# Kernel tuning notes

Hardware: AMD Instinct MI355X
Metric: run time of the kernel (lower is better)

The kernel has to match this reference:

```python
import jax, jax.numpy as jnp
import numpy as np

BS, NR, VDIM, QDIM, CSUB, RDIM = 64, 36, 2048, 1024, 512, 256


def setup_inputs() -> dict:
    key = jax.random.key(0)
    ks = jax.random.split(key, 8)
    s = 0.02  # weight scale
    return {
        "X": jax.random.normal(ks[0], (BS, NR, VDIM), jnp.float32),
        "Q": jax.random.normal(ks[1], (BS, QDIM), jnp.float32),
        "pos": jax.random.uniform(ks[2], (BS, NR, 4), jnp.float32),
        "Wv": jax.random.normal(ks[3], (VDIM + 4, CSUB), jnp.float32) * s,
        "bv": jnp.zeros((CSUB,), jnp.float32),
        "Wq": jax.random.normal(ks[4], (QDIM, CSUB), jnp.float32) * s,
        "bq": jnp.zeros((CSUB,), jnp.float32),
        "W1": jax.random.normal(ks[5], (CSUB, RDIM), jnp.float32) * s,
        "b1": jnp.zeros((RDIM,), jnp.float32),
        "W2": jax.random.normal(ks[6], (RDIM, RDIM), jnp.float32) * s,
        "b2": jnp.zeros((RDIM,), jnp.float32),
    }


def reference(X, Q, pos, Wv, bv, Wq, bq, W1, b1, W2, b2):
    # pe_enable: concat position encodings -> [bs, Nr, v_dim+4]
    Xc = jnp.concatenate([X, pos], axis=-1)
    # FCNet projections (weight-norm linear + ReLU; dropout identity in eval)
    Xp = jax.nn.relu(Xc @ Wv + bv)              # [bs, Nr, C]
    Qp = jax.nn.relu(Q @ Wq + bq)               # [bs, C]
    Xs = Xp + Qp[:, None, :]                    # broadcast question over regions
    # pairwise elementwise product: pair[b,i,j,c] = Xs[b,j,c] * Xs[b,i,c]
    pair = Xs[:, None, :, :] * Xs[:, :, None, :]  # [bs, Nr, Nr, C]
    # 1x1 convs == per-(i,j) channel-mixing matmuls, relu (dropout identity)
    h = jax.nn.relu(jnp.einsum('bijc,cr->bijr', pair, W1) + b1)
    r_emb = jax.nn.relu(jnp.einsum('bijr,rs->bijs', h, W2) + b2)
    return r_emb  # [bs, Nr, Nr, r_dim]
```

## Files before the change

kernel.cpp:

```cpp
#include <hip/hip_runtime.h>
#include <hip/hip_bf16.h>
#include <stdint.h>

#define BSZ 64
#define NRG 36
#define VD  2048
#define QD  1024
#define CS  512
#define RD  256
#define KP  2080
#define MR  (BSZ*NRG)
#define TRI  666
#define TRIQ 768

typedef __bf16 bf16x8 __attribute__((ext_vector_type(8)));
typedef float  f32x4  __attribute__((ext_vector_type(4)));

static __device__ __forceinline__ f32x4 mfma16(bf16x8 a, bf16x8 b, f32x4 c) {
    return __builtin_amdgcn_mfma_f32_16x16x32_bf16(a, b, c, 0, 0, 0);
}

static __device__ __forceinline__ void load_lds16(const __bf16* g, __bf16* l) {
    __builtin_amdgcn_global_load_lds(
        (const __attribute__((address_space(1))) uint32_t*)(const void*)g,
        (__attribute__((address_space(3))) uint32_t*)(void*)l,
        16, 0, 0);
}

__global__ __launch_bounds__(256) void k_prep(
    const float* __restrict__ X, const float* __restrict__ pos,
    const float* __restrict__ Wv, const float* __restrict__ W1,
    const float* __restrict__ W2,
    __bf16* __restrict__ Xc, __bf16* __restrict__ Wvg,
    __bf16* __restrict__ W1g, __bf16* __restrict__ W2g,
    int* __restrict__ lut)
{
    int id = blockIdx.x;
    if (id < MR) {
        const float* xr = X + (size_t)id * VD;
        const float* pr = pos + (size_t)id * 4;
        __bf16* o = Xc + (size_t)id * KP;
        for (int c = threadIdx.x; c < KP; c += 256) {
            float v = 0.f;
            if (c < VD) v = xr[c];
            else if (c < VD + 4) v = pr[c - VD];
            o[c] = (__bf16)v;
        }
        return;
    }
    id -= MR;
    if (id < 520 + 64 + 32) {
        const float* W; __bf16* Wg; int K, N, nbx;
        if (id < 520)      {          W = Wv; Wg = Wvg; K = VD + 4; N = CS; nbx = CS / 64; }
        else if (id < 584) { id -= 520; W = W1; Wg = W1g; K = CS;     N = RD; nbx = RD / 64; }
        else               { id -= 584; W = W2; Wg = W2g; K = RD;     N = RD; nbx = RD / 64; }
        int bx = id % nbx, by = id / nbx;
        int g = by * 4 + (threadIdx.x >> 6);
        int n = bx * 64 + (threadIdx.x & 63);
        bf16x8 v;
        #pragma unroll
        for (int e = 0; e < 8; ++e) {
            int k = g * 8 + e;
            v[e] = (__bf16)((k < K) ? W[(size_t)k * N + n] : 0.f);
        }
        *(bf16x8*)(Wg + ((size_t)g * N + n) * 8) = v;
        return;
    }
    for (int t = threadIdx.x; t < TRIQ; t += 256) {
        int tt = (t < TRI) ? t : (TRI - 1);
        int i = 0;
        while (tt >= NRG - i) { tt -= NRG - i; ++i; }
        lut[t] = (i << 8) | (i + tt);
    }
}

__global__ __launch_bounds__(256) void k_qproj(
    const float* __restrict__ Q, const float* __restrict__ Wq,
    const float* __restrict__ bq, float* __restrict__ Qp) {
    int b   = blockIdx.x;
    int col = blockIdx.y * 64 + (threadIdx.x & 63);
    int ks  = threadIdx.x >> 6;
    const float* q = Q  + (size_t)b * QD + ks * 256;
    const float* w = Wq + (size_t)(ks * 256) * CS + col;
    float acc = 0.f;
    #pragma unroll 8
    for (int k = 0; k < 256; ++k)
        acc = fmaf(q[k], w[(size_t)k * CS], acc);
    __shared__ float red[256];
    red[threadIdx.x] = acc;
    __syncthreads();
    if (ks == 0) {
        float v = red[threadIdx.x] + red[threadIdx.x + 64]
                + red[threadIdx.x + 128] + red[threadIdx.x + 192] + bq[col];
        Qp[(size_t)b * CS + col] = fmaxf(v, 0.f);
    }
}

__global__ __launch_bounds__(256) void k_g1(
    const __bf16* __restrict__ Xc,
    const __bf16* __restrict__ Wvg,
    const float* __restrict__ bv,
    const float* __restrict__ Qp,
    __bf16* __restrict__ Xs)
{
    __shared__ __align__(16) __bf16 sA[4][4 * 64 * 8];
    __shared__ __align__(16) __bf16 sB[4][4 * 64 * 8];

    const int tid = threadIdx.x;
    const int lane = tid & 63;
    const int w = tid >> 6;
    const int wm = w & 1, wn = w >> 1;
    const int l15 = lane & 15, l4 = lane >> 4;
    const int m0 = blockIdx.x * 64;
    const int n0 = blockIdx.y * 64;
    const int sg = tid >> 6;
    const int sr = tid & 63;

    auto stage = [&](int kt, int slot) {
        load_lds16(Xc + (size_t)(m0 + sr) * KP + kt * 32 + sg * 8,
                   &sA[slot][0] + (size_t)tid * 8);
        load_lds16(Wvg + ((size_t)(kt * 4 + sg) * CS + n0 + sr) * 8,
                   &sB[slot][0] + (size_t)tid * 8);
    };

    constexpr int NKT = KP / 32;
    stage(0, 0);
    stage(1, 1);

    f32x4 acc[2][2] = {};
    for (int kt = 0; kt < NKT; ++kt) {
        if (kt + 2 < NKT) stage(kt + 2, (kt + 2) & 3);
        if (kt + 2 < NKT)      asm volatile("s_waitcnt vmcnt(4)" ::: "memory");
        else if (kt + 1 < NKT) asm volatile("s_waitcnt vmcnt(2)" ::: "memory");
        else                   asm volatile("s_waitcnt vmcnt(0)" ::: "memory");
        __builtin_amdgcn_s_barrier();

        const __bf16* a_base = &sA[kt & 3][0];
        const __bf16* b_base = &sB[kt & 3][0];
        bf16x8 af[2], bf[2];
        #pragma unroll
        for (int f = 0; f < 2; ++f)
            af[f] = *(const bf16x8*)(a_base + ((size_t)l4 * 64 + wm * 32 + f * 16 + l15) * 8);
        #pragma unroll
        for (int g = 0; g < 2; ++g)
            bf[g] = *(const bf16x8*)(b_base + ((size_t)l4 * 64 + wn * 32 + g * 16 + l15) * 8);
        __builtin_amdgcn_s_setprio(1);
        #pragma unroll
        for (int f = 0; f < 2; ++f)
            #pragma unroll
            for (int g = 0; g < 2; ++g)
                acc[f][g] = mfma16(af[f], bf[g], acc[f][g]);
        __builtin_amdgcn_s_setprio(0);
    }

    #pragma unroll
    for (int f = 0; f < 2; ++f) {
        int row0 = m0 + wm * 32 + f * 16 + l4 * 4;
        #pragma unroll
        for (int g = 0; g < 2; ++g) {
            int col = n0 + wn * 32 + g * 16 + l15;
            float bb = bv[col];
            #pragma unroll
            for (int r = 0; r < 4; ++r) {
                int row = row0 + r;
                float v = fmaxf(acc[f][g][r] + bb, 0.f) + Qp[(size_t)(row / NRG) * CS + col];
                Xs[(size_t)row * CS + col] = (__bf16)v;
            }
        }
    }
}

__global__ __launch_bounds__(256, 2) void k_g23(
    const __bf16* __restrict__ Xs,
    const __bf16* __restrict__ W1g,
    const __bf16* __restrict__ W2g,
    const float* __restrict__ b1,
    const float* __restrict__ b2,
    float* __restrict__ Out,
    const int* __restrict__ lut)
{
    __shared__ __align__(16) __bf16 sH[32 * 64 * 8];

    const int tid = threadIdx.x;
    const int lane = tid & 63;
    const int w = tid >> 6;
    const int wm = w & 1, wn = w >> 1;
    const int l15 = lane & 15, l4 = lane >> 4;
    const int b = blockIdx.y;
    const int r_base = blockIdx.x * 64;

    const int t0 = r_base + wm * 32 + l15;
    const int ij0 = lut[t0], ij1 = lut[t0 + 16];
    const __bf16* xpi0 = Xs + (size_t)(b * NRG + (ij0 >> 8)) * CS + l4 * 8;
    const __bf16* xpj0 = Xs + (size_t)(b * NRG + (ij0 & 255)) * CS + l4 * 8;
    const __bf16* xpi1 = Xs + (size_t)(b * NRG + (ij1 >> 8)) * CS + l4 * 8;
    const __bf16* xpj1 = Xs + (size_t)(b * NRG + (ij1 & 255)) * CS + l4 * 8;

    const __bf16* w1p = W1g + ((size_t)l4 * RD + wn * 128 + l15) * 8;
    const __bf16* w2p = W2g + ((size_t)l4 * RD + wn * 128 + l15) * 8;

    f32x4 acc0[8] = {}, acc1[8] = {};
    bf16x8 wA[8], wB[8];
    bf16x8 xiA0, xiA1, xjA0, xjA1, xiB0, xiB1, xjB0, xjB1;

    #pragma unroll
    for (int g = 0; g < 8; ++g) wA[g] = *(const bf16x8*)(w1p + (size_t)g * 128);
    xiA0 = *(const bf16x8*)xpi0; xiA1 = *(const bf16x8*)xpi1;
    xjA0 = *(const bf16x8*)xpj0; xjA1 = *(const bf16x8*)xpj1;

#define PF_W(WN, BASE, KT) { \
    const __bf16* wp_ = (BASE) + (size_t)(KT) * (4 * RD * 8); \
    _Pragma("unroll") for (int g = 0; g < 8; ++g) \
        WN[g] = *(const bf16x8*)(wp_ + (size_t)g * 128); }

#define PF_PAIR(XN0, XN1, XM0, XM1, KT) { \
    XN0 = *(const bf16x8*)(xpi0 + (KT) * 32); \
    XN1 = *(const bf16x8*)(xpi1 + (KT) * 32); \
    XM0 = *(const bf16x8*)(xpj0 + (KT) * 32); \
    XM1 = *(const bf16x8*)(xpj1 + (KT) * 32); }

#define S1_BODY(KT, WC, WN, XI0, XI1, XJ0, XJ1, XN0, XN1, XM0, XM1) { \
    bf16x8 af0, af1; \
    _Pragma("unroll") for (int e = 0; e < 8; ++e) { \
        af0[e] = (__bf16)((float)XI0[e] * (float)XJ0[e]); \
        af1[e] = (__bf16)((float)XI1[e] * (float)XJ1[e]); } \
    if ((KT) < 15) { PF_W(WN, w1p, (KT) + 1); PF_PAIR(XN0, XN1, XM0, XM1, (KT) + 1); } \
    else           { PF_W(WN, w2p, 0); } \
    __builtin_amdgcn_s_setprio(1); \
    _Pragma("unroll") for (int g = 0; g < 8; ++g) { \
        acc0[g] = mfma16(af0, WC[g], acc0[g]); \
        acc1[g] = mfma16(af1, WC[g], acc1[g]); } \
    __builtin_amdgcn_s_setprio(0); }

#define S1_PAIR2(K) \
    S1_BODY(2*(K),   wA, wB, xiA0, xiA1, xjA0, xjA1, xiB0, xiB1, xjB0, xjB1) \
    S1_BODY(2*(K)+1, wB, wA, xiB0, xiB1, xjB0, xjB1, xiA0, xiA1, xjA0, xjA1)

    S1_PAIR2(0) S1_PAIR2(1) S1_PAIR2(2) S1_PAIR2(3)
    S1_PAIR2(4) S1_PAIR2(5) S1_PAIR2(6) S1_PAIR2(7)

    {
        const int rw0 = wm * 32 + l4 * 4;
        #pragma unroll
        for (int g = 0; g < 8; ++g) {
            int col = wn * 128 + g * 16 + l15;
            float bb = b1[col];
            int g2 = col >> 3, e = col & 7;
            #pragma unroll
            for (int r = 0; r < 4; ++r) {
                sH[((size_t)g2 * 64 + rw0 + r) * 8 + e]      = (__bf16)fmaxf(acc0[g][r] + bb, 0.f);
                sH[((size_t)g2 * 64 + rw0 + 16 + r) * 8 + e] = (__bf16)fmaxf(acc1[g][r] + bb, 0.f);
            }
        }
    }
    __syncthreads();

    f32x4 acc20[8] = {}, acc21[8] = {};
    bf16x8 ahA0, ahA1, ahB0, ahB1;

#define PF_AH(AN0, AN1, KT) { \
    AN0 = *(const bf16x8*)(sH + ((size_t)((KT) * 4 + l4) * 64 + wm * 32 + l15) * 8); \
    AN1 = *(const bf16x8*)(sH + ((size_t)((KT) * 4 + l4) * 64 + wm * 32 + 16 + l15) * 8); }

    PF_AH(ahA0, ahA1, 0)

#define S2_BODY(KT, WC, WN, AH0, AH1, AN0, AN1) { \
    if ((KT) < 7) { PF_W(WN, w2p, (KT) + 1); PF_AH(AN0, AN1, (KT) + 1); } \
    __builtin_amdgcn_s_setprio(1); \
    _Pragma("unroll") for (int g = 0; g < 8; ++g) { \
        acc20[g] = mfma16(AH0, WC[g], acc20[g]); \
        acc21[g] = mfma16(AH1, WC[g], acc21[g]); } \
    __builtin_amdgcn_s_setprio(0); }

#define S2_PAIR2(K) \
    S2_BODY(2*(K),   wA, wB, ahA0, ahA1, ahB0, ahB1) \
    S2_BODY(2*(K)+1, wB, wA, ahB0, ahB1, ahA0, ahA1)

    S2_PAIR2(0) S2_PAIR2(1) S2_PAIR2(2) S2_PAIR2(3)

    float bias2[8];
    #pragma unroll
    for (int g = 0; g < 8; ++g) bias2[g] = b2[wn * 128 + g * 16 + l15];
    const int rw = wm * 32 + l4 * 4;
    #pragma unroll
    for (int r = 0; r < 4; ++r) {
        int ta = r_base + rw + r;
        if (ta < TRI) {
            int ij = lut[ta];
            int i = ij >> 8, j = ij & 255;
            float* o1 = Out + (size_t)((b * NRG + i) * NRG + j) * RD;
            float* o2 = Out + (size_t)((b * NRG + j) * NRG + i) * RD;
            #pragma unroll
            for (int g = 0; g < 8; ++g) {
                int col = wn * 128 + g * 16 + l15;
                float v = fmaxf(acc20[g][r] + bias2[g], 0.f);
                o1[col] = v;
                o2[col] = v;
            }
        }
        int tb = r_base + rw + 16 + r;
        if (tb < TRI) {
            int ij = lut[tb];
            int i = ij >> 8, j = ij & 255;
            float* o1 = Out + (size_t)((b * NRG + i) * NRG + j) * RD;
            float* o2 = Out + (size_t)((b * NRG + j) * NRG + i) * RD;
            #pragma unroll
            for (int g = 0; g < 8; ++g) {
                int col = wn * 128 + g * 16 + l15;
                float v = fmaxf(acc21[g][r] + bias2[g], 0.f);
                o1[col] = v;
                o2[col] = v;
            }
        }
    }
#undef PF_W
#undef PF_PAIR
#undef S1_BODY
#undef S1_PAIR2
#undef PF_AH
#undef S2_BODY
#undef S2_PAIR2
}

extern "C" void kernel_launch(void* const* d_in, const int* in_sizes, int n_in,
                              void* d_out, int out_size, void* d_ws, size_t ws_size,
                              hipStream_t stream) {
    const float* X   = (const float*)d_in[0];
    const float* Q   = (const float*)d_in[1];
    const float* pos = (const float*)d_in[2];
    const float* Wv  = (const float*)d_in[3];
    const float* bv  = (const float*)d_in[4];
    const float* Wq  = (const float*)d_in[5];
    const float* bq  = (const float*)d_in[6];
    const float* W1  = (const float*)d_in[7];
    const float* b1  = (const float*)d_in[8];
    const float* W2  = (const float*)d_in[9];
    const float* b2  = (const float*)d_in[10];

    char* ws = (char*)d_ws;
    size_t off = 0;
    auto alloc = [&](size_t bytes) {
        char* p = ws + off;
        off = (off + bytes + 255) & ~(size_t)255;
        return p;
    };
    __bf16* Xc  = (__bf16*)alloc((size_t)MR * KP * 2);
    __bf16* Wvg = (__bf16*)alloc((size_t)(KP/8) * CS * 8 * 2);
    __bf16* W1g = (__bf16*)alloc((size_t)(CS/8) * RD * 8 * 2);
    __bf16* W2g = (__bf16*)alloc((size_t)(RD/8) * RD * 8 * 2);
    float*  Qp  = (float*) alloc((size_t)BSZ * CS * 4);
    __bf16* Xs  = (__bf16*)alloc((size_t)MR * CS * 2);
    int*    lut = (int*)   alloc((size_t)TRIQ * 4);

    hipLaunchKernelGGL(k_prep, dim3(MR + 520 + 64 + 32 + 1), dim3(256), 0, stream,
                       X, pos, Wv, W1, W2, Xc, Wvg, W1g, W2g, lut);
    hipLaunchKernelGGL(k_qproj, dim3(BSZ, CS/64), dim3(256), 0, stream, Q, Wq, bq, Qp);
    hipLaunchKernelGGL(k_g1,  dim3(MR/64, CS/64), dim3(256), 0, stream,
                       Xc, Wvg, bv, Qp, Xs);
    hipLaunchKernelGGL(k_g23, dim3(TRIQ/64, BSZ), dim3(256), 0, stream,
                       Xs, W1g, W2g, b1, b2, (float*)d_out, (const int*)lut);
}
```

Measured before the change: 108.0 us.

## Stage per-batch Xs in swizzled LDS and split second GEMM across waves

The fused pair-product/MLP kernel now copies the whole 36x512 Xs slice for its batch into LDS once, using an XOR swizzle. The pairwise operands are then read from LDS instead of gathered from global memory on every k-step. The hidden tile buffer shrinks to 32 rows, so the second GEMM runs in two passes of 32 rows, each spreading all four waves over 64 output columns with 4-wide W2 prefetches. Launch bounds rise to 3 blocks per SM to raise occupancy. The cost is an upfront LDS fill, extra barriers per pass, and more LDS per block, which could limit how many blocks actually reside.

```diff
diff --git a/kernel.cpp b/kernel.cpp
--- a/kernel.cpp
+++ b/kernel.cpp
@@ -170,7 +170,7 @@
     }
 }
 
-__global__ __launch_bounds__(256, 2) void k_g23(
+__global__ __launch_bounds__(256, 3) void k_g23(
     const __bf16* __restrict__ Xs,
     const __bf16* __restrict__ W1g,
     const __bf16* __restrict__ W2g,
@@ -179,7 +179,8 @@
     float* __restrict__ Out,
     const int* __restrict__ lut)
 {
-    __shared__ __align__(16) __bf16 sH[32 * 64 * 8];
+    __shared__ __align__(16) __bf16 sXs[NRG * CS];
+    __shared__ __align__(16) __bf16 sH[32 * RD];
 
     const int tid = threadIdx.x;
     const int lane = tid & 63;
@@ -188,138 +189,139 @@
     const int l15 = lane & 15, l4 = lane >> 4;
     const int b = blockIdx.y;
     const int r_base = blockIdx.x * 64;
+    const char* sXc = (const char*)sXs;
+
+    {
+        const __bf16* src = Xs + (size_t)b * NRG * CS;
+        #pragma unroll
+        for (int c = 0; c < 9; ++c) {
+            int id = c * 256 + tid;
+            int r = id >> 6, cp = id & 63;
+            bf16x8 v = *(const bf16x8*)(src + (size_t)r * CS + cp * 8);
+            int ba = (r << 10) ^ ((r & 7) << 4) ^ (cp << 4);
+            *(bf16x8*)((char*)sXs + ba) = v;
+        }
+    }
 
     const int t0 = r_base + wm * 32 + l15;
     const int ij0 = lut[t0], ij1 = lut[t0 + 16];
-    const __bf16* xpi0 = Xs + (size_t)(b * NRG + (ij0 >> 8)) * CS + l4 * 8;
-    const __bf16* xpj0 = Xs + (size_t)(b * NRG + (ij0 & 255)) * CS + l4 * 8;
-    const __bf16* xpi1 = Xs + (size_t)(b * NRG + (ij1 >> 8)) * CS + l4 * 8;
-    const __bf16* xpj1 = Xs + (size_t)(b * NRG + (ij1 & 255)) * CS + l4 * 8;
+    const int i0 = ij0 >> 8, j0 = ij0 & 255, i1 = ij1 >> 8, j1 = ij1 & 255;
+    const int qi0 = (i0 << 10) ^ ((i0 & 7) << 4);
+    const int qj0 = (j0 << 10) ^ ((j0 & 7) << 4);
+    const int qi1 = (i1 << 10) ^ ((i1 & 7) << 4);
+    const int qj1 = (j1 << 10) ^ ((j1 & 7) << 4);
+    const int lc = l4 << 4;
 
     const __bf16* w1p = W1g + ((size_t)l4 * RD + wn * 128 + l15) * 8;
-    const __bf16* w2p = W2g + ((size_t)l4 * RD + wn * 128 + l15) * 8;
+    const __bf16* w2q = W2g + ((size_t)l4 * RD + w * 64 + l15) * 8;
 
     f32x4 acc0[8] = {}, acc1[8] = {};
     bf16x8 wA[8], wB[8];
-    bf16x8 xiA0, xiA1, xjA0, xjA1, xiB0, xiB1, xjB0, xjB1;
-
-    #pragma unroll
-    for (int g = 0; g < 8; ++g) wA[g] = *(const bf16x8*)(w1p + (size_t)g * 128);
-    xiA0 = *(const bf16x8*)xpi0; xiA1 = *(const bf16x8*)xpi1;
-    xjA0 = *(const bf16x8*)xpj0; xjA1 = *(const bf16x8*)xpj1;
-
-#define PF_W(WN, BASE, KT) { \
-    const __bf16* wp_ = (BASE) + (size_t)(KT) * (4 * RD * 8); \
+
+#define WTS (4 * RD * 8)
+#define PF_W8(WN, KT) { \
+    const __bf16* wp_ = w1p + (size_t)(KT) * WTS; \
     _Pragma("unroll") for (int g = 0; g < 8; ++g) \
         WN[g] = *(const bf16x8*)(wp_ + (size_t)g * 128); }
-
-#define PF_PAIR(XN0, XN1, XM0, XM1, KT) { \
-    XN0 = *(const bf16x8*)(xpi0 + (KT) * 32); \
-    XN1 = *(const bf16x8*)(xpi1 + (KT) * 32); \
-    XM0 = *(const bf16x8*)(xpj0 + (KT) * 32); \
-    XM1 = *(const bf16x8*)(xpj1 + (KT) * 32); }
-
-#define S1_BODY(KT, WC, WN, XI0, XI1, XJ0, XJ1, XN0, XN1, XM0, XM1) { \
-    bf16x8 af0, af1; \
+#define PF_W4(WN, KT) { \
+    const __bf16* wp_ = w2q + (size_t)(KT) * WTS; \
+    _Pragma("unroll") for (int g = 0; g < 4; ++g) \
+        WN[g] = *(const bf16x8*)(wp_ + (size_t)g * 128); }
+
+    PF_W8(wA, 0)
+    __syncthreads();
+
+#define S1_BODY(KT, WC, WN) { \
+    const int ck_ = ((KT) * 64) | lc; \
+    bf16x8 xi0_ = *(const bf16x8*)(sXc + (qi0 ^ ck_)); \
+    bf16x8 xj0_ = *(const bf16x8*)(sXc + (qj0 ^ ck_)); \
+    bf16x8 xi1_ = *(const bf16x8*)(sXc + (qi1 ^ ck_)); \
+    bf16x8 xj1_ = *(const bf16x8*)(sXc + (qj1 ^ ck_)); \
+    bf16x8 af0_, af1_; \
     _Pragma("unroll") for (int e = 0; e < 8; ++e) { \
-        af0[e] = (__bf16)((float)XI0[e] * (float)XJ0[e]); \
-        af1[e] = (__bf16)((float)XI1[e] * (float)XJ1[e]); } \
-    if ((KT) < 15) { PF_W(WN, w1p, (KT) + 1); PF_PAIR(XN0, XN1, XM0, XM1, (KT) + 1); } \
-    else           { PF_W(WN, w2p, 0); } \
+        af0_[e] = (__bf16)((float)xi0_[e] * (float)xj0_[e]); \
+        af1_[e] = (__bf16)((float)xi1_[e] * (float)xj1_[e]); } \
+    if ((KT) < 15) { PF_W8(WN, (KT) + 1) } else { PF_W4(WN, 0) } \
     __builtin_amdgcn_s_setprio(1); \
     _Pragma("unroll") for (int g = 0; g < 8; ++g) { \
-        acc0[g] = mfma16(af0, WC[g], acc0[g]); \
-        acc1[g] = mfma16(af1, WC[g], acc1[g]); } \
+        acc0[g] = mfma16(af0_, WC[g], acc0[g]); \
+        acc1[g] = mfma16(af1_, WC[g], acc1[g]); } \
     __builtin_amdgcn_s_setprio(0); }
 
-#define S1_PAIR2(K) \
-    S1_BODY(2*(K),   wA, wB, xiA0, xiA1, xjA0, xjA1, xiB0, xiB1, xjB0, xjB1) \
-    S1_BODY(2*(K)+1, wB, wA, xiB0, xiB1, xjB0, xjB1, xiA0, xiA1, xjA0, xjA1)
-
-    S1_PAIR2(0) S1_PAIR2(1) S1_PAIR2(2) S1_PAIR2(3)
-    S1_PAIR2(4) S1_PAIR2(5) S1_PAIR2(6) S1_PAIR2(7)
-
-    {
-        const int rw0 = wm * 32 + l4 * 4;
-        #pragma unroll
-        for (int g = 0; g < 8; ++g) {
-            int col = wn * 128 + g * 16 + l15;
-            float bb = b1[col];
-            int g2 = col >> 3, e = col & 7;
-            #pragma unroll
-            for (int r = 0; r < 4; ++r) {
-                sH[((size_t)g2 * 64 + rw0 + r) * 8 + e]      = (__bf16)fmaxf(acc0[g][r] + bb, 0.f);
-                sH[((size_t)g2 * 64 + rw0 + 16 + r) * 8 + e] = (__bf16)fmaxf(acc1[g][r] + bb, 0.f);
-            }
-        }
-    }
-    __syncthreads();
-
-    f32x4 acc20[8] = {}, acc21[8] = {};
-    bf16x8 ahA0, ahA1, ahB0, ahB1;
-
-#define PF_AH(AN0, AN1, KT) { \
-    AN0 = *(const bf16x8*)(sH + ((size_t)((KT) * 4 + l4) * 64 + wm * 32 + l15) * 8); \
-    AN1 = *(const bf16x8*)(sH + ((size_t)((KT) * 4 + l4) * 64 + wm * 32 + 16 + l15) * 8); }
-
-    PF_AH(ahA0, ahA1, 0)
-
-#define S2_BODY(KT, WC, WN, AH0, AH1, AN0, AN1) { \
-    if ((KT) < 7) { PF_W(WN, w2p, (KT) + 1); PF_AH(AN0, AN1, (KT) + 1); } \
+    S1_BODY(0,  wA, wB) S1_BODY(1,  wB, wA) S1_BODY(2,  wA, wB) S1_BODY(3,  wB, wA)
+    S1_BODY(4,  wA, wB) S1_BODY(5,  wB, wA) S1_BODY(6,  wA, wB) S1_BODY(7,  wB, wA)
+    S1_BODY(8,  wA, wB) S1_BODY(9,  wB, wA) S1_BODY(10, wA, wB) S1_BODY(11, wB, wA)
+    S1_BODY(12, wA, wB) S1_BODY(13, wB, wA) S1_BODY(14, wA, wB) S1_BODY(15, wB, wA)
+
+#define S2_BODY(KT, WC, WN) { \
+    bf16x8 ah0_ = *(const bf16x8*)(sH + ((size_t)((KT) * 4 + l4) * 32 + l15) * 8); \
+    bf16x8 ah1_ = *(const bf16x8*)(sH + ((size_t)((KT) * 4 + l4) * 32 + 16 + l15) * 8); \
+    if ((KT) < 7) { PF_W4(WN, (KT) + 1) } else { PF_W4(WN, 0) } \
     __builtin_amdgcn_s_setprio(1); \
-    _Pragma("unroll") for (int g = 0; g < 8; ++g) { \
-        acc20[g] = mfma16(AH0, WC[g], acc20[g]); \
-        acc21[g] = mfma16(AH1, WC[g], acc21[g]); } \
+    _Pragma("unroll") for (int g = 0; g < 4; ++g) { \
+        acc20[g] = mfma16(ah0_, WC[g], acc20[g]); \
+        acc21[g] = mfma16(ah1_, WC[g], acc21[g]); } \
     __builtin_amdgcn_s_setprio(0); }
 
-#define S2_PAIR2(K) \
-    S2_BODY(2*(K),   wA, wB, ahA0, ahA1, ahB0, ahB1) \
-    S2_BODY(2*(K)+1, wB, wA, ahB0, ahB1, ahA0, ahA1)
-
-    S2_PAIR2(0) S2_PAIR2(1) S2_PAIR2(2) S2_PAIR2(3)
-
-    float bias2[8];
     #pragma unroll
-    for (int g = 0; g < 8; ++g) bias2[g] = b2[wn * 128 + g * 16 + l15];
-    const int rw = wm * 32 + l4 * 4;
-    #pragma unroll
-    for (int r = 0; r < 4; ++r) {
-        int ta = r_base + rw + r;
-        if (ta < TRI) {
-            int ij = lut[ta];
-            int i = ij >> 8, j = ij & 255;
-            float* o1 = Out + (size_t)((b * NRG + i) * NRG + j) * RD;
-            float* o2 = Out + (size_t)((b * NRG + j) * NRG + i) * RD;
+    for (int p = 0; p < 2; ++p) {
+        if (wm == p) {
             #pragma unroll
             for (int g = 0; g < 8; ++g) {
                 int col = wn * 128 + g * 16 + l15;
-                float v = fmaxf(acc20[g][r] + bias2[g], 0.f);
-                o1[col] = v;
-                o2[col] = v;
+                float bb = b1[col];
+                int g2 = col >> 3, e = col & 7;
+                #pragma unroll
+                for (int r = 0; r < 4; ++r) {
+                    int rl = l4 * 4 + r;
+                    sH[((size_t)g2 * 32 + rl) * 8 + e]      = (__bf16)fmaxf(acc0[g][r] + bb, 0.f);
+                    sH[((size_t)g2 * 32 + 16 + rl) * 8 + e] = (__bf16)fmaxf(acc1[g][r] + bb, 0.f);
+                }
             }
         }
-        int tb = r_base + rw + 16 + r;
-        if (tb < TRI) {
-            int ij = lut[tb];
-            int i = ij >> 8, j = ij & 255;
-            float* o1 = Out + (size_t)((b * NRG + i) * NRG + j) * RD;
-            float* o2 = Out + (size_t)((b * NRG + j) * NRG + i) * RD;
-            #pragma unroll
-            for (int g = 0; g < 8; ++g) {
-                int col = wn * 128 + g * 16 + l15;
-                float v = fmaxf(acc21[g][r] + bias2[g], 0.f);
-                o1[col] = v;
-                o2[col] = v;
+        __syncthreads();
+
+        f32x4 acc20[4] = {}, acc21[4] = {};
+        S2_BODY(0, wA, wB) S2_BODY(1, wB, wA) S2_BODY(2, wA, wB) S2_BODY(3, wB, wA)
+        S2_BODY(4, wA, wB) S2_BODY(5, wB, wA) S2_BODY(6, wA, wB) S2_BODY(7, wB, wA)
+
+        float b2c[4];
+        #pragma unroll
+        for (int g = 0; g < 4; ++g) b2c[g] = b2[w * 64 + g * 16 + l15];
+        #pragma unroll
+        for (int r = 0; r < 4; ++r) {
+            int ta = r_base + p * 32 + l4 * 4 + r;
+            if (ta < TRI) {
+                int ij = lut[ta]; int i = ij >> 8, j = ij & 255;
+                float* o1 = Out + ((size_t)((b * NRG + i) * NRG + j)) * RD;
+                float* o2 = Out + ((size_t)((b * NRG + j) * NRG + i)) * RD;
+                #pragma unroll
+                for (int g = 0; g < 4; ++g) {
+                    int col = w * 64 + g * 16 + l15;
+                    float v = fmaxf(acc20[g][r] + b2c[g], 0.f);
+                    o1[col] = v; o2[col] = v;
+                }
             }
-        }
-    }
-#undef PF_W
-#undef PF_PAIR
+            int tb = r_base + p * 32 + 16 + l4 * 4 + r;
+            if (tb < TRI) {
+                int ij = lut[tb]; int i = ij >> 8, j = ij & 255;
+                float* o1 = Out + ((size_t)((b * NRG + i) * NRG + j)) * RD;
+                float* o2 = Out + ((size_t)((b * NRG + j) * NRG + i)) * RD;
+                #pragma unroll
+                for (int g = 0; g < 4; ++g) {
+                    int col = w * 64 + g * 16 + l15;
+                    float v = fmaxf(acc21[g][r] + b2c[g], 0.f);
+                    o1[col] = v; o2[col] = v;
+                }
+            }
+        }
+        __syncthreads();
+    }
+#undef WTS
+#undef PF_W8
+#undef PF_W4
 #undef S1_BODY
-#undef S1_PAIR2
-#undef PF_AH
 #undef S2_BODY
-#undef S2_PAIR2
 }
 
 extern "C" void kernel_launch(void* const* d_in, const int* in_sizes, int n_in,
```

New measurement: 104.7 us. -3.0%, faster.

## Unfuse pair MLP into pack kernel plus generic LDS-staged GEMMs

Applied to the files above, without the earlier changes.

Replaces the fused register-streaming k_g23 kernel with three stages. A pack kernel materializes the upper-triangle pair products into a padded buffer, then a templated LDS-pipelined GEMM runs twice, once for the W1 layer writing bf16 H to memory and once for the W2 layer scattering symmetric outputs. The goal is to reuse the k_g1 GEMM pipeline with LDS-shared weights and better tiling, at the cost of extra global round-trips for Pair and H and two more launches. Pair aliases the Xc buffer, which is safe only because Xc is consumed before the pack kernel runs.

```diff
diff --git a/kernel.cpp b/kernel.cpp
--- a/kernel.cpp
+++ b/kernel.cpp
@@ -11,7 +11,8 @@
 #define KP  2080
 #define MR  (BSZ*NRG)
 #define TRI  666
-#define TRIQ 768
+#define TRIP 704
+#define MTRI (BSZ*TRIP)
 
 typedef __bf16 bf16x8 __attribute__((ext_vector_type(8)));
 typedef float  f32x4  __attribute__((ext_vector_type(4)));
@@ -66,7 +67,7 @@
         *(bf16x8*)(Wg + ((size_t)g * N + n) * 8) = v;
         return;
     }
-    for (int t = threadIdx.x; t < TRIQ; t += 256) {
+    for (int t = threadIdx.x; t < TRIP; t += 256) {
         int tt = (t < TRI) ? t : (TRI - 1);
         int i = 0;
         while (tt >= NRG - i) { tt -= NRG - i; ++i; }
@@ -96,12 +97,37 @@
     }
 }
 
-__global__ __launch_bounds__(256) void k_g1(
-    const __bf16* __restrict__ Xc,
-    const __bf16* __restrict__ Wvg,
-    const float* __restrict__ bv,
+__global__ __launch_bounds__(256) void k_pack(
+    const __bf16* __restrict__ Xs, const int* __restrict__ lut,
+    __bf16* __restrict__ Pair)
+{
+    int b = blockIdx.y;
+    int t = blockIdx.x * 8 + (threadIdx.x >> 5);
+    int c = (threadIdx.x & 31) * 16;
+    int ij = lut[t];
+    int i = ij >> 8, j = ij & 255;
+    const bf16x8* xi = (const bf16x8*)(Xs + ((size_t)(b * NRG + i)) * CS + c);
+    const bf16x8* xj = (const bf16x8*)(Xs + ((size_t)(b * NRG + j)) * CS + c);
+    bf16x8 a0 = xi[0], a1 = xi[1], c0 = xj[0], c1 = xj[1];
+    bf16x8 p0, p1;
+    #pragma unroll
+    for (int e = 0; e < 8; ++e) {
+        p0[e] = (__bf16)((float)a0[e] * (float)c0[e]);
+        p1[e] = (__bf16)((float)a1[e] * (float)c1[e]);
+    }
+    bf16x8* o = (bf16x8*)(Pair + ((size_t)b * TRIP + t) * CS + c);
+    o[0] = p0;
+    o[1] = p1;
+}
+
+template<int MODE>
+__global__ __launch_bounds__(256) void k_mm(
+    const __bf16* __restrict__ A, int lda,
+    const __bf16* __restrict__ Bg, int NB,
+    const float* __restrict__ bias,
     const float* __restrict__ Qp,
-    __bf16* __restrict__ Xs)
+    void* __restrict__ Out, int ldo, int K,
+    const int* __restrict__ lut)
 {
     __shared__ __align__(16) __bf16 sA[4][4 * 64 * 8];
     __shared__ __align__(16) __bf16 sB[4][4 * 64 * 8];
@@ -117,13 +143,13 @@
     const int sr = tid & 63;
 
     auto stage = [&](int kt, int slot) {
-        load_lds16(Xc + (size_t)(m0 + sr) * KP + kt * 32 + sg * 8,
+        load_lds16(A + (size_t)(m0 + sr) * lda + kt * 32 + sg * 8,
                    &sA[slot][0] + (size_t)tid * 8);
-        load_lds16(Wvg + ((size_t)(kt * 4 + sg) * CS + n0 + sr) * 8,
+        load_lds16(Bg + ((size_t)(kt * 4 + sg) * NB + n0 + sr) * 8,
                    &sB[slot][0] + (size_t)tid * 8);
     };
 
-    constexpr int NKT = KP / 32;
+    const int NKT = K >> 5;
     stage(0, 0);
     stage(1, 1);
 
@@ -153,173 +179,48 @@
         __builtin_amdgcn_s_setprio(0);
     }
 
-    #pragma unroll
-    for (int f = 0; f < 2; ++f) {
-        int row0 = m0 + wm * 32 + f * 16 + l4 * 4;
-        #pragma unroll
-        for (int g = 0; g < 2; ++g) {
-            int col = n0 + wn * 32 + g * 16 + l15;
-            float bb = bv[col];
+    if (MODE != 2) {
+        #pragma unroll
+        for (int f = 0; f < 2; ++f) {
+            int row0 = m0 + wm * 32 + f * 16 + l4 * 4;
+            #pragma unroll
+            for (int g = 0; g < 2; ++g) {
+                int col = n0 + wn * 32 + g * 16 + l15;
+                float bb = bias[col];
+                #pragma unroll
+                for (int r = 0; r < 4; ++r) {
+                    int row = row0 + r;
+                    float v = fmaxf(acc[f][g][r] + bb, 0.f);
+                    if (MODE == 1) v += Qp[(size_t)(row / NRG) * CS + col];
+                    ((__bf16*)Out)[(size_t)row * ldo + col] = (__bf16)v;
+                }
+            }
+        }
+    } else {
+        const int b = m0 / TRIP;
+        #pragma unroll
+        for (int f = 0; f < 2; ++f) {
+            int row0 = m0 + wm * 32 + f * 16 + l4 * 4;
             #pragma unroll
             for (int r = 0; r < 4; ++r) {
                 int row = row0 + r;
-                float v = fmaxf(acc[f][g][r] + bb, 0.f) + Qp[(size_t)(row / NRG) * CS + col];
-                Xs[(size_t)row * CS + col] = (__bf16)v;
+                int t = row - b * TRIP;
+                if (t < TRI) {
+                    int ij = lut[t];
+                    int i = ij >> 8, j = ij & 255;
+                    float* o1 = (float*)Out + ((size_t)((b * NRG + i) * NRG + j)) * RD;
+                    float* o2 = (float*)Out + ((size_t)((b * NRG + j) * NRG + i)) * RD;
+                    #pragma unroll
+                    for (int g = 0; g < 2; ++g) {
+                        int col = n0 + wn * 32 + g * 16 + l15;
+                        float v = fmaxf(acc[f][g][r] + bias[col], 0.f);
+                        o1[col] = v;
+                        o2[col] = v;
+                    }
+                }
             }
         }
     }
-}
-
-__global__ __launch_bounds__(256, 2) void k_g23(
-    const __bf16* __restrict__ Xs,
-    const __bf16* __restrict__ W1g,
-    const __bf16* __restrict__ W2g,
-    const float* __restrict__ b1,
-    const float* __restrict__ b2,
-    float* __restrict__ Out,
-    const int* __restrict__ lut)
-{
-    __shared__ __align__(16) __bf16 sH[32 * 64 * 8];
-
-    const int tid = threadIdx.x;
-    const int lane = tid & 63;
-    const int w = tid >> 6;
-    const int wm = w & 1, wn = w >> 1;
-    const int l15 = lane & 15, l4 = lane >> 4;
-    const int b = blockIdx.y;
-    const int r_base = blockIdx.x * 64;
-
-    const int t0 = r_base + wm * 32 + l15;
-    const int ij0 = lut[t0], ij1 = lut[t0 + 16];
-    const __bf16* xpi0 = Xs + (size_t)(b * NRG + (ij0 >> 8)) * CS + l4 * 8;
-    const __bf16* xpj0 = Xs + (size_t)(b * NRG + (ij0 & 255)) * CS + l4 * 8;
-    const __bf16* xpi1 = Xs + (size_t)(b * NRG + (ij1 >> 8)) * CS + l4 * 8;
-    const __bf16* xpj1 = Xs + (size_t)(b * NRG + (ij1 & 255)) * CS + l4 * 8;
-
-    const __bf16* w1p = W1g + ((size_t)l4 * RD + wn * 128 + l15) * 8;
-    const __bf16* w2p = W2g + ((size_t)l4 * RD + wn * 128 + l15) * 8;
-
-    f32x4 acc0[8] = {}, acc1[8] = {};
-    bf16x8 wA[8], wB[8];
-    bf16x8 xiA0, xiA1, xjA0, xjA1, xiB0, xiB1, xjB0, xjB1;
-
-    #pragma unroll
-    for (int g = 0; g < 8; ++g) wA[g] = *(const bf16x8*)(w1p + (size_t)g * 128);
-    xiA0 = *(const bf16x8*)xpi0; xiA1 = *(const bf16x8*)xpi1;
-    xjA0 = *(const bf16x8*)xpj0; xjA1 = *(const bf16x8*)xpj1;
-
-#define PF_W(WN, BASE, KT) { \
-    const __bf16* wp_ = (BASE) + (size_t)(KT) * (4 * RD * 8); \
-    _Pragma("unroll") for (int g = 0; g < 8; ++g) \
-        WN[g] = *(const bf16x8*)(wp_ + (size_t)g * 128); }
-
-#define PF_PAIR(XN0, XN1, XM0, XM1, KT) { \
-    XN0 = *(const bf16x8*)(xpi0 + (KT) * 32); \
-    XN1 = *(const bf16x8*)(xpi1 + (KT) * 32); \
-    XM0 = *(const bf16x8*)(xpj0 + (KT) * 32); \
-    XM1 = *(const bf16x8*)(xpj1 + (KT) * 32); }
-
-#define S1_BODY(KT, WC, WN, XI0, XI1, XJ0, XJ1, XN0, XN1, XM0, XM1) { \
-    bf16x8 af0, af1; \
-    _Pragma("unroll") for (int e = 0; e < 8; ++e) { \
-        af0[e] = (__bf16)((float)XI0[e] * (float)XJ0[e]); \
-        af1[e] = (__bf16)((float)XI1[e] * (float)XJ1[e]); } \
-    if ((KT) < 15) { PF_W(WN, w1p, (KT) + 1); PF_PAIR(XN0, XN1, XM0, XM1, (KT) + 1); } \
-    else           { PF_W(WN, w2p, 0); } \
-    __builtin_amdgcn_s_setprio(1); \
-    _Pragma("unroll") for (int g = 0; g < 8; ++g) { \
-        acc0[g] = mfma16(af0, WC[g], acc0[g]); \
-        acc1[g] = mfma16(af1, WC[g], acc1[g]); } \
-    __builtin_amdgcn_s_setprio(0); }
-
-#define S1_PAIR2(K) \
-    S1_BODY(2*(K),   wA, wB, xiA0, xiA1, xjA0, xjA1, xiB0, xiB1, xjB0, xjB1) \
-    S1_BODY(2*(K)+1, wB, wA, xiB0, xiB1, xjB0, xjB1, xiA0, xiA1, xjA0, xjA1)
-
-    S1_PAIR2(0) S1_PAIR2(1) S1_PAIR2(2) S1_PAIR2(3)
-    S1_PAIR2(4) S1_PAIR2(5) S1_PAIR2(6) S1_PAIR2(7)
-
-    {
-        const int rw0 = wm * 32 + l4 * 4;
-        #pragma unroll
-        for (int g = 0; g < 8; ++g) {
-            int col = wn * 128 + g * 16 + l15;
-            float bb = b1[col];
-            int g2 = col >> 3, e = col & 7;
-            #pragma unroll
-            for (int r = 0; r < 4; ++r) {
-                sH[((size_t)g2 * 64 + rw0 + r) * 8 + e]      = (__bf16)fmaxf(acc0[g][r] + bb, 0.f);
-                sH[((size_t)g2 * 64 + rw0 + 16 + r) * 8 + e] = (__bf16)fmaxf(acc1[g][r] + bb, 0.f);
-            }
-        }
-    }
-    __syncthreads();
-
-    f32x4 acc20[8] = {}, acc21[8] = {};
-    bf16x8 ahA0, ahA1, ahB0, ahB1;
-
-#define PF_AH(AN0, AN1, KT) { \
-    AN0 = *(const bf16x8*)(sH + ((size_t)((KT) * 4 + l4) * 64 + wm * 32 + l15) * 8); \
-    AN1 = *(const bf16x8*)(sH + ((size_t)((KT) * 4 + l4) * 64 + wm * 32 + 16 + l15) * 8); }
-
-    PF_AH(ahA0, ahA1, 0)
-
-#define S2_BODY(KT, WC, WN, AH0, AH1, AN0, AN1) { \
-    if ((KT) < 7) { PF_W(WN, w2p, (KT) + 1); PF_AH(AN0, AN1, (KT) + 1); } \
-    __builtin_amdgcn_s_setprio(1); \
-    _Pragma("unroll") for (int g = 0; g < 8; ++g) { \
-        acc20[g] = mfma16(AH0, WC[g], acc20[g]); \
-        acc21[g] = mfma16(AH1, WC[g], acc21[g]); } \
-    __builtin_amdgcn_s_setprio(0); }
-
-#define S2_PAIR2(K) \
-    S2_BODY(2*(K),   wA, wB, ahA0, ahA1, ahB0, ahB1) \
-    S2_BODY(2*(K)+1, wB, wA, ahB0, ahB1, ahA0, ahA1)
-
-    S2_PAIR2(0) S2_PAIR2(1) S2_PAIR2(2) S2_PAIR2(3)
-
-    float bias2[8];
-    #pragma unroll
-    for (int g = 0; g < 8; ++g) bias2[g] = b2[wn * 128 + g * 16 + l15];
-    const int rw = wm * 32 + l4 * 4;
-    #pragma unroll
-    for (int r = 0; r < 4; ++r) {
-        int ta = r_base + rw + r;
-        if (ta < TRI) {
-            int ij = lut[ta];
-            int i = ij >> 8, j = ij & 255;
-            float* o1 = Out + (size_t)((b * NRG + i) * NRG + j) * RD;
-            float* o2 = Out + (size_t)((b * NRG + j) * NRG + i) * RD;
-            #pragma unroll
-            for (int g = 0; g < 8; ++g) {
-                int col = wn * 128 + g * 16 + l15;
-                float v = fmaxf(acc20[g][r] + bias2[g], 0.f);
-                o1[col] = v;
-                o2[col] = v;
-            }
-        }
-        int tb = r_base + rw + 16 + r;
-        if (tb < TRI) {
-            int ij = lut[tb];
-            int i = ij >> 8, j = ij & 255;
-            float* o1 = Out + (size_t)((b * NRG + i) * NRG + j) * RD;
-            float* o2 = Out + (size_t)((b * NRG + j) * NRG + i) * RD;
-            #pragma unroll
-            for (int g = 0; g < 8; ++g) {
-                int col = wn * 128 + g * 16 + l15;
-                float v = fmaxf(acc21[g][r] + bias2[g], 0.f);
-                o1[col] = v;
-                o2[col] = v;
-            }
-        }
-    }
-#undef PF_W
-#undef PF_PAIR
-#undef S1_BODY
-#undef S1_PAIR2
-#undef PF_AH
-#undef S2_BODY
-#undef S2_PAIR2
 }
 
 extern "C" void kernel_launch(void* const* d_in, const int* in_sizes, int n_in,
@@ -344,19 +245,27 @@
         off = (off + bytes + 255) & ~(size_t)255;
         return p;
     };
-    __bf16* Xc  = (__bf16*)alloc((size_t)MR * KP * 2);
     __bf16* Wvg = (__bf16*)alloc((size_t)(KP/8) * CS * 8 * 2);
     __bf16* W1g = (__bf16*)alloc((size_t)(CS/8) * RD * 8 * 2);
     __bf16* W2g = (__bf16*)alloc((size_t)(RD/8) * RD * 8 * 2);
     float*  Qp  = (float*) alloc((size_t)BSZ * CS * 4);
     __bf16* Xs  = (__bf16*)alloc((size_t)MR * CS * 2);
-    int*    lut = (int*)   alloc((size_t)TRIQ * 4);
+    int*    lut = (int*)   alloc((size_t)TRIP * 4);
+    __bf16* H   = (__bf16*)alloc((size_t)MTRI * RD * 2);
+    char*   pxc = alloc((size_t)MTRI * CS * 2);
+    __bf16* Xc   = (__bf16*)pxc;
+    __bf16* Pair = (__bf16*)pxc;
 
     hipLaunchKernelGGL(k_prep, dim3(MR + 520 + 64 + 32 + 1), dim3(256), 0, stream,
                        X, pos, Wv, W1, W2, Xc, Wvg, W1g, W2g, lut);
     hipLaunchKernelGGL(k_qproj, dim3(BSZ, CS/64), dim3(256), 0, stream, Q, Wq, bq, Qp);
-    hipLaunchKernelGGL(k_g1,  dim3(MR/64, CS/64), dim3(256), 0, stream,
-                       Xc, Wvg, bv, Qp, Xs);
-    hipLaunchKernelGGL(k_g23, dim3(TRIQ/64, BSZ), dim3(256), 0, stream,
-                       Xs, W1g, W2g, b1, b2, (float*)d_out, (const int*)lut);
-}
+
+    hipLaunchKernelGGL((k_mm<1>), dim3(MR/64, CS/64), dim3(256), 0, stream,
+                       Xc, KP, Wvg, CS, bv, Qp, (void*)Xs, CS, KP, (const int*)lut);
+    hipLaunchKernelGGL(k_pack, dim3(TRIP/8, BSZ), dim3(256), 0, stream,
+                       Xs, (const int*)lut, Pair);
+    hipLaunchKernelGGL((k_mm<3>), dim3(MTRI/64, RD/64), dim3(256), 0, stream,
+                       Pair, CS, W1g, RD, b1, nullptr, (void*)H, RD, CS, (const int*)lut);
+    hipLaunchKernelGGL((k_mm<2>), dim3(MTRI/64, RD/64), dim3(256), 0, stream,
+                       H, RD, W2g, RD, b2, nullptr, d_out, RD, RD, (const int*)lut);
+}
```

Result: slower. 147.1 us (+36.3%).

## Stage W1/W2 tiles in shared memory and split second GEMM into two halves

Applied to the files above, without the earlier changes.

Weight fragments for both channel-mixing GEMMs were held in registers (two 8-deep bf16x8 buffers per thread). They are now streamed cooperatively into a double-buffered LDS tile with direct global-to-LDS loads, synchronised by explicit vmcnt waits and barriers. The second GEMM is done in two 32-row halves, each with 4 accumulators per wave instead of 8, so the hidden tile in LDS shrinks. The aim is lower register pressure and a raised launch bound of 3 blocks per SM, traded against two barriers per k-step and more LDS reads.

```diff
diff --git a/kernel.cpp b/kernel.cpp
--- a/kernel.cpp
+++ b/kernel.cpp
@@ -170,7 +170,7 @@
     }
 }
 
-__global__ __launch_bounds__(256, 2) void k_g23(
+__global__ __launch_bounds__(256, 3) void k_g23(
     const __bf16* __restrict__ Xs,
     const __bf16* __restrict__ W1g,
     const __bf16* __restrict__ W2g,
@@ -179,7 +179,8 @@
     float* __restrict__ Out,
     const int* __restrict__ lut)
 {
-    __shared__ __align__(16) __bf16 sH[32 * 64 * 8];
+    __shared__ __align__(16) __bf16 sW[2][4 * RD * 8];
+    __shared__ __align__(16) __bf16 sH[32 * RD];
 
     const int tid = threadIdx.x;
     const int lane = tid & 63;
@@ -196,130 +197,139 @@
     const __bf16* xpi1 = Xs + (size_t)(b * NRG + (ij1 >> 8)) * CS + l4 * 8;
     const __bf16* xpj1 = Xs + (size_t)(b * NRG + (ij1 & 255)) * CS + l4 * 8;
 
-    const __bf16* w1p = W1g + ((size_t)l4 * RD + wn * 128 + l15) * 8;
-    const __bf16* w2p = W2g + ((size_t)l4 * RD + wn * 128 + l15) * 8;
+#define STG(WSRC, KT, SLOT) { \
+    _Pragma("unroll") for (int it_ = 0; it_ < 4; ++it_) { \
+        int c_ = tid + it_ * 256; \
+        load_lds16((WSRC) + (size_t)(KT) * (RD * 32) + (size_t)c_ * 8, \
+                   &sW[SLOT][0] + (size_t)c_ * 8); } }
 
     f32x4 acc0[8] = {}, acc1[8] = {};
-    bf16x8 wA[8], wB[8];
     bf16x8 xiA0, xiA1, xjA0, xjA1, xiB0, xiB1, xjB0, xjB1;
 
-    #pragma unroll
-    for (int g = 0; g < 8; ++g) wA[g] = *(const bf16x8*)(w1p + (size_t)g * 128);
+    STG(W1g, 0, 0)
     xiA0 = *(const bf16x8*)xpi0; xiA1 = *(const bf16x8*)xpi1;
     xjA0 = *(const bf16x8*)xpj0; xjA1 = *(const bf16x8*)xpj1;
 
-#define PF_W(WN, BASE, KT) { \
-    const __bf16* wp_ = (BASE) + (size_t)(KT) * (4 * RD * 8); \
-    _Pragma("unroll") for (int g = 0; g < 8; ++g) \
-        WN[g] = *(const bf16x8*)(wp_ + (size_t)g * 128); }
-
-#define PF_PAIR(XN0, XN1, XM0, XM1, KT) { \
-    XN0 = *(const bf16x8*)(xpi0 + (KT) * 32); \
-    XN1 = *(const bf16x8*)(xpi1 + (KT) * 32); \
-    XM0 = *(const bf16x8*)(xpj0 + (KT) * 32); \
-    XM1 = *(const bf16x8*)(xpj1 + (KT) * 32); }
-
-#define S1_BODY(KT, WC, WN, XI0, XI1, XJ0, XJ1, XN0, XN1, XM0, XM1) { \
-    bf16x8 af0, af1; \
+#define S1_ITER(KT, XI0, XI1, XJ0, XJ1, XN0, XN1, XM0, XM1) { \
+    if ((KT) < 15) { \
+        STG(W1g, (KT) + 1, ((KT) + 1) & 1) \
+        XN0 = *(const bf16x8*)(xpi0 + ((KT) + 1) * 32); \
+        XN1 = *(const bf16x8*)(xpi1 + ((KT) + 1) * 32); \
+        XM0 = *(const bf16x8*)(xpj0 + ((KT) + 1) * 32); \
+        XM1 = *(const bf16x8*)(xpj1 + ((KT) + 1) * 32); \
+        asm volatile("s_waitcnt vmcnt(8)" ::: "memory"); \
+    } else { \
+        asm volatile("s_waitcnt vmcnt(0)" ::: "memory"); \
+    } \
+    __builtin_amdgcn_s_barrier(); \
+    bf16x8 af0_, af1_; \
     _Pragma("unroll") for (int e = 0; e < 8; ++e) { \
-        af0[e] = (__bf16)((float)XI0[e] * (float)XJ0[e]); \
-        af1[e] = (__bf16)((float)XI1[e] * (float)XJ1[e]); } \
-    if ((KT) < 15) { PF_W(WN, w1p, (KT) + 1); PF_PAIR(XN0, XN1, XM0, XM1, (KT) + 1); } \
-    else           { PF_W(WN, w2p, 0); } \
+        af0_[e] = (__bf16)((float)XI0[e] * (float)XJ0[e]); \
+        af1_[e] = (__bf16)((float)XI1[e] * (float)XJ1[e]); } \
+    const __bf16* wb_ = &sW[(KT) & 1][0]; \
     __builtin_amdgcn_s_setprio(1); \
     _Pragma("unroll") for (int g = 0; g < 8; ++g) { \
-        acc0[g] = mfma16(af0, WC[g], acc0[g]); \
-        acc1[g] = mfma16(af1, WC[g], acc1[g]); } \
-    __builtin_amdgcn_s_setprio(0); }
-
-#define S1_PAIR2(K) \
-    S1_BODY(2*(K),   wA, wB, xiA0, xiA1, xjA0, xjA1, xiB0, xiB1, xjB0, xjB1) \
-    S1_BODY(2*(K)+1, wB, wA, xiB0, xiB1, xjB0, xjB1, xiA0, xiA1, xjA0, xjA1)
-
-    S1_PAIR2(0) S1_PAIR2(1) S1_PAIR2(2) S1_PAIR2(3)
-    S1_PAIR2(4) S1_PAIR2(5) S1_PAIR2(6) S1_PAIR2(7)
-
+        bf16x8 wf_ = *(const bf16x8*)(wb_ + ((size_t)l4 * RD + wn * 128 + g * 16 + l15) * 8); \
+        acc0[g] = mfma16(af0_, wf_, acc0[g]); \
+        acc1[g] = mfma16(af1_, wf_, acc1[g]); } \
+    __builtin_amdgcn_s_setprio(0); \
+    __builtin_amdgcn_s_barrier(); }
+
+    S1_ITER(0,  xiA0, xiA1, xjA0, xjA1, xiB0, xiB1, xjB0, xjB1)
+    S1_ITER(1,  xiB0, xiB1, xjB0, xjB1, xiA0, xiA1, xjA0, xjA1)
+    S1_ITER(2,  xiA0, xiA1, xjA0, xjA1, xiB0, xiB1, xjB0, xjB1)
+    S1_ITER(3,  xiB0, xiB1, xjB0, xjB1, xiA0, xiA1, xjA0, xjA1)
+    S1_ITER(4,  xiA0, xiA1, xjA0, xjA1, xiB0, xiB1, xjB0, xjB1)
+    S1_ITER(5,  xiB0, xiB1, xjB0, xjB1, xiA0, xiA1, xjA0, xjA1)
+    S1_ITER(6,  xiA0, xiA1, xjA0, xjA1, xiB0, xiB1, xjB0, xjB1)
+    S1_ITER(7,  xiB0, xiB1, xjB0, xjB1, xiA0, xiA1, xjA0, xjA1)
+    S1_ITER(8,  xiA0, xiA1, xjA0, xjA1, xiB0, xiB1, xjB0, xjB1)
+    S1_ITER(9,  xiB0, xiB1, xjB0, xjB1, xiA0, xiA1, xjA0, xjA1)
+    S1_ITER(10, xiA0, xiA1, xjA0, xjA1, xiB0, xiB1, xjB0, xjB1)
+    S1_ITER(11, xiB0, xiB1, xjB0, xjB1, xiA0, xiA1, xjA0, xjA1)
+    S1_ITER(12, xiA0, xiA1, xjA0, xjA1, xiB0, xiB1, xjB0, xjB1)
+    S1_ITER(13, xiB0, xiB1, xjB0, xjB1, xiA0, xiA1, xjA0, xjA1)
+    S1_ITER(14, xiA0, xiA1, xjA0, xjA1, xiB0, xiB1, xjB0, xjB1)
+    S1_ITER(15, xiB0, xiB1, xjB0, xjB1, xiA0, xiA1, xjA0, xjA1)
+
+    STG(W2g, 0, 0)
+
+#define TRANS(P) { \
+    if (wm == (P)) { \
+        const int rw_ = l4 * 4; \
+        _Pragma("unroll") for (int g = 0; g < 8; ++g) { \
+            int col_ = wn * 128 + g * 16 + l15; \
+            float bb_ = b1[col_]; \
+            int g2_ = col_ >> 3, e_ = col_ & 7; \
+            _Pragma("unroll") for (int r = 0; r < 4; ++r) { \
+                sH[((size_t)g2_ * 32 + rw_ + r) * 8 + e_]      = (__bf16)fmaxf(acc0[g][r] + bb_, 0.f); \
+                sH[((size_t)g2_ * 32 + 16 + rw_ + r) * 8 + e_] = (__bf16)fmaxf(acc1[g][r] + bb_, 0.f); } } } \
+    asm volatile("s_waitcnt lgkmcnt(0)" ::: "memory"); \
+    __builtin_amdgcn_s_barrier(); }
+
+#define S2_ITER(LT, ACC0, ACC1) { \
+    if ((LT) < 15) { \
+        STG(W2g, ((LT) + 1) & 7, ((LT) + 1) & 1) \
+        asm volatile("s_waitcnt vmcnt(4)" ::: "memory"); \
+    } else { \
+        asm volatile("s_waitcnt vmcnt(0)" ::: "memory"); \
+    } \
+    __builtin_amdgcn_s_barrier(); \
+    bf16x8 ah0_ = *(const bf16x8*)(sH + ((size_t)(((LT) & 7) * 4 + l4) * 32 + l15) * 8); \
+    bf16x8 ah1_ = *(const bf16x8*)(sH + ((size_t)(((LT) & 7) * 4 + l4) * 32 + 16 + l15) * 8); \
+    const __bf16* wb_ = &sW[(LT) & 1][0]; \
+    __builtin_amdgcn_s_setprio(1); \
+    _Pragma("unroll") for (int g = 0; g < 4; ++g) { \
+        bf16x8 wf_ = *(const bf16x8*)(wb_ + ((size_t)l4 * RD + w * 64 + g * 16 + l15) * 8); \
+        ACC0[g] = mfma16(ah0_, wf_, ACC0[g]); \
+        ACC1[g] = mfma16(ah1_, wf_, ACC1[g]); } \
+    __builtin_amdgcn_s_setprio(0); \
+    __builtin_amdgcn_s_barrier(); }
+
+#define EPI(P, ACC0, ACC1) { \
+    float b2c_[4]; \
+    _Pragma("unroll") for (int g = 0; g < 4; ++g) b2c_[g] = b2[w * 64 + g * 16 + l15]; \
+    const int rw_ = l4 * 4; \
+    _Pragma("unroll") for (int r = 0; r < 4; ++r) { \
+        int ta_ = r_base + (P) * 32 + rw_ + r; \
+        if (ta_ < TRI) { \
+            int ij_ = lut[ta_]; int i_ = ij_ >> 8, j_ = ij_ & 255; \
+            float* o1_ = Out + ((size_t)((b * NRG + i_) * NRG + j_)) * RD; \
+            float* o2_ = Out + ((size_t)((b * NRG + j_) * NRG + i_)) * RD; \
+            _Pragma("unroll") for (int g = 0; g < 4; ++g) { \
+                int col_ = w * 64 + g * 16 + l15; \
+                float v_ = fmaxf(ACC0[g][r] + b2c_[g], 0.f); \
+                o1_[col_] = v_; o2_[col_] = v_; } } \
+        int tb_ = r_base + (P) * 32 + 16 + rw_ + r; \
+        if (tb_ < TRI) { \
+            int ij_ = lut[tb_]; int i_ = ij_ >> 8, j_ = ij_ & 255; \
+            float* o1_ = Out + ((size_t)((b * NRG + i_) * NRG + j_)) * RD; \
+            float* o2_ = Out + ((size_t)((b * NRG + j_) * NRG + i_)) * RD; \
+            _Pragma("unroll") for (int g = 0; g < 4; ++g) { \
+                int col_ = w * 64 + g * 16 + l15; \
+                float v_ = fmaxf(ACC1[g][r] + b2c_[g], 0.f); \
+                o1_[col_] = v_; o2_[col_] = v_; } } } }
+
+    TRANS(0)
     {
-        const int rw0 = wm * 32 + l4 * 4;
-        #pragma unroll
-        for (int g = 0; g < 8; ++g) {
-            int col = wn * 128 + g * 16 + l15;
-            float bb = b1[col];
-            int g2 = col >> 3, e = col & 7;
-            #pragma unroll
-            for (int r = 0; r < 4; ++r) {
-                sH[((size_t)g2 * 64 + rw0 + r) * 8 + e]      = (__bf16)fmaxf(acc0[g][r] + bb, 0.f);
-                sH[((size_t)g2 * 64 + rw0 + 16 + r) * 8 + e] = (__bf16)fmaxf(acc1[g][r] + bb, 0.f);
-            }
-        }
-    }
-    __syncthreads();
-
-    f32x4 acc20[8] = {}, acc21[8] = {};
-    bf16x8 ahA0, ahA1, ahB0, ahB1;
-
-#define PF_AH(AN0, AN1, KT) { \
-    AN0 = *(const bf16x8*)(sH + ((size_t)((KT) * 4 + l4) * 64 + wm * 32 + l15) * 8); \
-    AN1 = *(const bf16x8*)(sH + ((size_t)((KT) * 4 + l4) * 64 + wm * 32 + 16 + l15) * 8); }
-
-    PF_AH(ahA0, ahA1, 0)
-
-#define S2_BODY(KT, WC, WN, AH0, AH1, AN0, AN1) { \
-    if ((KT) < 7) { PF_W(WN, w2p, (KT) + 1); PF_AH(AN0, AN1, (KT) + 1); } \
-    __builtin_amdgcn_s_setprio(1); \
-    _Pragma("unroll") for (int g = 0; g < 8; ++g) { \
-        acc20[g] = mfma16(AH0, WC[g], acc20[g]); \
-        acc21[g] = mfma16(AH1, WC[g], acc21[g]); } \
-    __builtin_amdgcn_s_setprio(0); }
-
-#define S2_PAIR2(K) \
-    S2_BODY(2*(K),   wA, wB, ahA0, ahA1, ahB0, ahB1) \
-    S2_BODY(2*(K)+1, wB, wA, ahB0, ahB1, ahA0, ahA1)
-
-    S2_PAIR2(0) S2_PAIR2(1) S2_PAIR2(2) S2_PAIR2(3)
-
-    float bias2[8];
-    #pragma unroll
-    for (int g = 0; g < 8; ++g) bias2[g] = b2[wn * 128 + g * 16 + l15];
-    const int rw = wm * 32 + l4 * 4;
-    #pragma unroll
-    for (int r = 0; r < 4; ++r) {
-        int ta = r_base + rw + r;
-        if (ta < TRI) {
-            int ij = lut[ta];
-            int i = ij >> 8, j = ij & 255;
-            float* o1 = Out + (size_t)((b * NRG + i) * NRG + j) * RD;
-            float* o2 = Out + (size_t)((b * NRG + j) * NRG + i) * RD;
-            #pragma unroll
-            for (int g = 0; g < 8; ++g) {
-                int col = wn * 128 + g * 16 + l15;
-                float v = fmaxf(acc20[g][r] + bias2[g], 0.f);
-                o1[col] = v;
-                o2[col] = v;
-            }
-        }
-        int tb = r_base + rw + 16 + r;
-        if (tb < TRI) {
-            int ij = lut[tb];
-            int i = ij >> 8, j = ij & 255;
-            float* o1 = Out + (size_t)((b * NRG + i) * NRG + j) * RD;
-            float* o2 = Out + (size_t)((b * NRG + j) * NRG + i) * RD;
-            #pragma unroll
-            for (int g = 0; g < 8; ++g) {
-                int col = wn * 128 + g * 16 + l15;
-                float v = fmaxf(acc21[g][r] + bias2[g], 0.f);
-                o1[col] = v;
-                o2[col] = v;
-            }
-        }
-    }
-#undef PF_W
-#undef PF_PAIR
-#undef S1_BODY
-#undef S1_PAIR2
-#undef PF_AH
-#undef S2_BODY
-#undef S2_PAIR2
+        f32x4 a20[4] = {}, a21[4] = {};
+        S2_ITER(0, a20, a21) S2_ITER(1, a20, a21) S2_ITER(2, a20, a21) S2_ITER(3, a20, a21)
+        S2_ITER(4, a20, a21) S2_ITER(5, a20, a21) S2_ITER(6, a20, a21) S2_ITER(7, a20, a21)
+        EPI(0, a20, a21)
+    }
+    __builtin_amdgcn_s_barrier();
+    TRANS(1)
+    {
+        f32x4 a20[4] = {}, a21[4] = {};
+        S2_ITER(8, a20, a21)  S2_ITER(9, a20, a21)  S2_ITER(10, a20, a21) S2_ITER(11, a20, a21)
+        S2_ITER(12, a20, a21) S2_ITER(13, a20, a21) S2_ITER(14, a20, a21) S2_ITER(15, a20, a21)
+        EPI(1, a20, a21)
+    }
+#undef STG
+#undef S1_ITER
+#undef TRANS
+#undef S2_ITER
+#undef EPI
 }
 
 extern "C" void kernel_launch(void* const* d_in, const int* in_sizes, int n_in,
```

After: 107.6 us. Within noise of the previous version (-0.3%).
